# Kernel optimization log

Measured on AMD Instinct MI355X. Metric: run time of the kernel, lower is better.

Reference implementation:

```python
import jax, jax.numpy as jnp
import numpy as np

B, S, D, H, FF = 4, 2048, 512, 8, 2048
HD = D // H
SCALE = float(D) ** 0.5  # original scales by sqrt(embed_dim), not sqrt(head_dim)
EPS = 1e-5


def setup_inputs() -> dict:
    key = jax.random.key(0)
    ks = jax.random.split(key, 16)
    s_in = 1.0 / np.sqrt(D)
    s_ff = 1.0 / np.sqrt(FF)
    return {
        "embeddings": jax.random.normal(ks[0], (B, S, D), dtype=jnp.float32),
        "mask": jnp.ones((B, S), dtype=bool),
        # per-head Q/K/V projections stacked: [H, D, HD]
        "Wq": jax.random.uniform(ks[1], (H, D, HD), jnp.float32, -s_in, s_in),
        "bq": jax.random.uniform(ks[2], (H, HD), jnp.float32, -s_in, s_in),
        "Wk": jax.random.uniform(ks[3], (H, D, HD), jnp.float32, -s_in, s_in),
        "bk": jax.random.uniform(ks[4], (H, HD), jnp.float32, -s_in, s_in),
        "Wv": jax.random.uniform(ks[5], (H, D, HD), jnp.float32, -s_in, s_in),
        "bv": jax.random.uniform(ks[6], (H, HD), jnp.float32, -s_in, s_in),
        "Wc": jax.random.uniform(ks[7], (D, D), jnp.float32, -s_in, s_in),
        "bc": jax.random.uniform(ks[8], (D,), jnp.float32, -s_in, s_in),
        "W1": jax.random.uniform(ks[9], (D, FF), jnp.float32, -s_in, s_in),
        "b1": jax.random.uniform(ks[10], (FF,), jnp.float32, -s_in, s_in),
        "W2": jax.random.uniform(ks[11], (FF, D), jnp.float32, -s_ff, s_ff),
        "b2": jax.random.uniform(ks[12], (D,), jnp.float32, -s_ff, s_ff),
        "gamma": jnp.ones((D,), jnp.float32),
        "beta": jnp.zeros((D,), jnp.float32),
    }


def reference(embeddings, mask, Wq, bq, Wk, bk, Wv, bv, Wc, bc, W1, b1, W2, b2, gamma, beta):
    # Per-head projections batched into one einsum each: [B,H,S,HD]
    Q = jnp.einsum("bsd,hdf->bhsf", embeddings, Wq) + bq[:, None, :]
    K = jnp.einsum("bsd,hdf->bhsf", embeddings, Wk) + bk[:, None, :]
    V = jnp.einsum("bsd,hdf->bhsf", embeddings, Wv) + bv[:, None, :]
    # NOTE: the original computes a masked score tensor but then softmaxes the
    # UNMASKED scores (bug). We faithfully ignore the mask here.
    scores = jnp.einsum("bhsf,bhtf->bhst", Q, K) / SCALE  # [B,H,S,S]
    A = jax.nn.softmax(scores, axis=-1)
    Hh = jnp.einsum("bhst,bhtf->bhsf", A, V)  # [B,H,S,HD]
    # concat heads along feature dim (head h -> contiguous slice)
    Hcat = jnp.transpose(Hh, (0, 2, 1, 3)).reshape(B, S, D)
    Hp = Hcat @ Wc + bc
    # add & norm (dropout is identity at eval)
    res = Hp + embeddings
    mu = jnp.mean(res, axis=-1, keepdims=True)
    var = jnp.var(res, axis=-1, keepdims=True)
    Hn = (res - mu) / jnp.sqrt(var + EPS) * gamma + beta
    out = jax.nn.relu(Hn @ W1 + b1) @ W2 + b2  # no residual after FFN in original
    return out, mask
```

## Files before the change

### kernel.cpp

```cpp
#include <hip/hip_runtime.h>
#include <hip/hip_bf16.h>
#include <cstdint>
#include <cstddef>

typedef short  s16x8 __attribute__((ext_vector_type(8)));
typedef short  s16x4 __attribute__((ext_vector_type(4)));
typedef float  f32x4 __attribute__((ext_vector_type(4)));
typedef unsigned u32x2 __attribute__((ext_vector_type(2)));

static constexpr int Bb = 4, Ss = 2048, Dd = 512, Hh = 8, HDd = 64, FFf = 2048;
static constexpr int Mm = Bb * Ss;

__device__ __forceinline__ unsigned short f2bf(float f) {
  unsigned u = __float_as_uint(f);
  u += 0x7FFFu + ((u >> 16) & 1u);
  return (unsigned short)(u >> 16);
}

__device__ __forceinline__ unsigned cvt_pk_bf16(float lo, float hi) {
  unsigned r;
  asm("v_cvt_pk_bf16_f32 %0, %1, %2" : "=v"(r) : "v"(lo), "v"(hi));
  return r;
}

#define GLOAD_LDS16(gp, lp)                                                     \
  __builtin_amdgcn_global_load_lds((const __attribute__((address_space(1))) void*)(gp), \
                                   (__attribute__((address_space(3))) void*)(lp), 16, 0, 0)

__device__ __forceinline__ void xpose_tile(const float* __restrict__ in,
                                           unsigned short* __restrict__ out,
                                           int K, int N, int bx, int by, float (*t)[33]) {
  const int lx = threadIdx.x & 31, ly = threadIdx.x >> 5;
  const int n0 = bx * 32, k0 = by * 32;
#pragma unroll
  for (int r = 0; r < 4; ++r) t[ly + r * 8][lx] = in[(size_t)(k0 + ly + r * 8) * N + n0 + lx];
  __syncthreads();
#pragma unroll
  for (int r = 0; r < 4; ++r)
    out[(size_t)(n0 + ly + r * 8) * K + k0 + lx] = f2bf(t[lx][ly + r * 8]);
}

__global__ __launch_bounds__(256) void prep_all(
    const float* __restrict__ emb, const float* __restrict__ Wq, const float* __restrict__ Wk,
    const float* __restrict__ Wv, const float* __restrict__ Wc, const float* __restrict__ W1,
    const float* __restrict__ W2, unsigned short* __restrict__ embB,
    unsigned short* __restrict__ WtQKV, unsigned short* __restrict__ WtC,
    unsigned short* __restrict__ Wt1, unsigned short* __restrict__ Wt2,
    float* __restrict__ maskOut) {
  __shared__ float t[32][33];
  const int blk = blockIdx.x;
  if (blk < 4096) {
    const int i = blk * 256 + threadIdx.x;
    const float4 v = reinterpret_cast<const float4*>(emb)[i];
    s16x4 o; o[0] = f2bf(v.x); o[1] = f2bf(v.y); o[2] = f2bf(v.z); o[3] = f2bf(v.w);
    reinterpret_cast<s16x4*>(embB)[i] = o;
  } else if (blk < 4864) {
    const int b = blk - 4096;
    const int bx = b & 15, by = (b >> 4) & 1, z = b >> 5;
    const int sel = z >> 3, h = z & 7;
    const float* W = sel == 0 ? Wq : (sel == 1 ? Wk : Wv);
    const float* inb = W + (size_t)h * 512 * 64;
    unsigned short* outb = WtQKV + (size_t)sel * 512 * 512 + (size_t)h * 64 * 512;
    const int lx = threadIdx.x & 31, ly = threadIdx.x >> 5;
    const int d0 = bx * 32, f0 = by * 32;
#pragma unroll
    for (int r = 0; r < 4; ++r) t[ly + r * 8][lx] = inb[(size_t)(d0 + ly + r * 8) * 64 + f0 + lx];
    __syncthreads();
#pragma unroll
    for (int r = 0; r < 4; ++r)
      outb[(size_t)(f0 + ly + r * 8) * 512 + d0 + lx] = f2bf(t[lx][ly + r * 8]);
  } else if (blk < 5120) {
    const int b = blk - 4864;
    xpose_tile(Wc, WtC, 512, 512, b & 15, b >> 4, t);
  } else if (blk < 6144) {
    const int b = blk - 5120;
    xpose_tile(W1, Wt1, 512, 2048, b & 63, b >> 6, t);
  } else if (blk < 7168) {
    const int b = blk - 6144;
    xpose_tile(W2, Wt2, 2048, 512, b & 15, b >> 4, t);
  } else {
    const int i = (blk - 7168) * 256 + threadIdx.x;
    if (i < Bb * Ss) maskOut[i] = 1.0f;
  }
}

template<int EPI>
__global__ __launch_bounds__(256) void gemm_bt(
    const unsigned short* __restrict__ A, const unsigned short* __restrict__ Bt,
    const float* __restrict__ bias0, const float* __restrict__ bias1, const float* __restrict__ bias2,
    const float* __restrict__ addf, float* __restrict__ outF,
    unsigned short* __restrict__ outB0, unsigned short* __restrict__ outB1,
    unsigned short* __restrict__ outB2, int M, int N, int K) {
  __shared__ alignas(16) unsigned short As[2][128 * 32];
  __shared__ alignas(16) unsigned short Bs[2][128 * 32];
  const int tid = threadIdx.x;
  const int lane = tid & 63, wid = tid >> 6;
  const int wr = wid >> 1, wc = wid & 1;
  const int fr = lane & 15, kg = lane >> 4;
  const int m0 = blockIdx.y * 128, n0 = blockIdx.x * 128;

  const unsigned short* gA = A + (size_t)(m0 + (tid >> 2)) * K + ((tid & 3) << 3);
  const unsigned short* gB = Bt + (size_t)(n0 + (tid >> 2)) * K + ((tid & 3) << 3);

  auto STAGE = [&](int kt, int buf) {
    unsigned short* lA = &As[buf][wid * 512];
    unsigned short* lB = &Bs[buf][wid * 512];
    GLOAD_LDS16(gA + kt, lA);
    GLOAD_LDS16(gA + (size_t)64 * K + kt, lA + 2048);
    GLOAD_LDS16(gB + kt, lB);
    GLOAD_LDS16(gB + (size_t)64 * K + kt, lB + 2048);
  };

  f32x4 acc[4][4];
#pragma unroll
  for (int i = 0; i < 4; ++i)
#pragma unroll
    for (int j = 0; j < 4; ++j)
#pragma unroll
      for (int r = 0; r < 4; ++r) acc[i][j][r] = 0.f;

  STAGE(0, 0);
  const int nk = K >> 5;
  for (int ki = 0; ki < nk; ++ki) {
    const int cur = ki & 1;
    __builtin_amdgcn_s_barrier();
    if (ki + 1 < nk) {
      STAGE((ki + 1) << 5, cur ^ 1);
      asm volatile("s_waitcnt vmcnt(4)" ::: "memory");
    } else {
      asm volatile("s_waitcnt vmcnt(0)" ::: "memory");
    }
    __builtin_amdgcn_sched_barrier(0);
    __builtin_amdgcn_s_barrier();
    __builtin_amdgcn_sched_barrier(0);

    s16x8 af[4], bfv[4];
#pragma unroll
    for (int i = 0; i < 4; ++i)
      af[i] = *reinterpret_cast<const s16x8*>(&As[cur][(wr * 64 + i * 16 + fr) * 32 + kg * 8]);
#pragma unroll
    for (int i = 0; i < 4; ++i)
      bfv[i] = *reinterpret_cast<const s16x8*>(&Bs[cur][(wc * 64 + i * 16 + fr) * 32 + kg * 8]);
#pragma unroll
    for (int mi = 0; mi < 4; ++mi)
#pragma unroll
      for (int ni = 0; ni < 4; ++ni)
        acc[mi][ni] = __builtin_amdgcn_mfma_f32_16x16x32_bf16(af[mi], bfv[ni], acc[mi][ni], 0, 0, 0);
  }

#pragma unroll
  for (int mi = 0; mi < 4; ++mi)
#pragma unroll
    for (int ni = 0; ni < 4; ++ni)
#pragma unroll
      for (int r = 0; r < 4; ++r) {
        const int row = m0 + wr * 64 + mi * 16 + kg * 4 + r;
        const int col = n0 + wc * 64 + ni * 16 + fr;
        float v = acc[mi][ni][r];
        if constexpr (EPI == 0) {
          const int sel = col >> 9, c = col & 511;
          const float* bs = sel == 0 ? bias0 : (sel == 1 ? bias1 : bias2);
          v += bs[c];
          const int b = row >> 11, s = row & 2047;
          const int h = c >> 6, f = c & 63;
          if (sel == 0)
            outB0[((size_t)((b << 3) + h) * 2048 + s) * 64 + f] = f2bf(v);
          else if (sel == 1)
            outB1[((size_t)((b << 3) + h) * 2048 + s) * 64 + f] = f2bf(v);
          else
            outB2[((size_t)((b << 3) + h) * 64 + f) * 2048 + s] = f2bf(v);
        } else if constexpr (EPI == 1) {
          const size_t idx = (size_t)row * 512 + col;
          outF[idx] = v + bias0[col] + addf[idx];
        } else if constexpr (EPI == 2) {
          v += bias0[col];
          outB0[(size_t)row * 2048 + col] = f2bf(v > 0.f ? v : 0.f);
        } else {
          outF[(size_t)row * 512 + col] = v + bias0[col];
        }
      }
}

__global__ __launch_bounds__(256) void attn_kernel(const unsigned short* __restrict__ Q,
                                                   const unsigned short* __restrict__ Kx,
                                                   const unsigned short* __restrict__ V,
                                                   unsigned short* __restrict__ Hcat) {
  const int lane = threadIdx.x & 63, wid = threadIdx.x >> 6;
  const int fr = lane & 15, kg = lane >> 4;
  const int lin = blockIdx.x;
  const int xcd = lin & 7, idx = lin >> 3;
  const int bh = xcd * 4 + (idx & 3);
  const int qi = idx >> 2;
  const int b = bh >> 3, h = bh & 7;
  const int q0 = qi * 64 + wid * 16;
  const unsigned short* Qh = Q + (size_t)bh * Ss * HDd;
  const unsigned short* Kh = Kx + (size_t)bh * Ss * HDd;
  const unsigned short* Vh = V + (size_t)bh * HDd * Ss;

  __shared__ alignas(16) unsigned short Ks[2][64 * 64];
  __shared__ alignas(16) unsigned short Vs[64 * 64];
  __shared__ alignas(16) unsigned short P[4][16][72];

  const int srow = lane >> 3;
  const int scol = ((lane & 7) ^ srow) << 3;
  const unsigned short* gK0 = Kh + (size_t)(8 * (2 * wid + 0) + srow) * 64 + scol;
  const unsigned short* gK1 = Kh + (size_t)(8 * (2 * wid + 1) + srow) * 64 + scol;
  const unsigned short* gV0 = Vh + (size_t)(8 * (2 * wid + 0) + srow) * 2048 + scol;
  const unsigned short* gV1 = Vh + (size_t)(8 * (2 * wid + 1) + srow) * 2048 + scol;
  unsigned short* lK0a = &Ks[0][(2 * wid + 0) * 512];
  unsigned short* lK1a = &Ks[0][(2 * wid + 1) * 512];
  unsigned short* lK0b = &Ks[1][(2 * wid + 0) * 512];
  unsigned short* lK1b = &Ks[1][(2 * wid + 1) * 512];
  unsigned short* lV0 = &Vs[(2 * wid + 0) * 512];
  unsigned short* lV1 = &Vs[(2 * wid + 1) * 512];

  s16x8 bq[2];
#pragma unroll
  for (int kb = 0; kb < 2; ++kb)
    bq[kb] = *reinterpret_cast<const s16x8*>(&Qh[(size_t)(q0 + fr) * 64 + kb * 32 + kg * 8]);

  f32x4 o[4];
#pragma unroll
  for (int ct = 0; ct < 4; ++ct)
#pragma unroll
    for (int r = 0; r < 4; ++r) o[ct][r] = 0.f;
  float mr = -1e30f, lsum = 0.f;

  const float iscL = 1.4426950408889634f * 0.044194173824159216f;
  const int swz = (fr & 7) << 3;

  GLOAD_LDS16(gK0, lK0a);
  GLOAD_LDS16(gK1, lK1a);
  GLOAD_LDS16(gV0, lV0);
  GLOAD_LDS16(gV1, lV1);

#pragma unroll 1
  for (int t = 0; t < 32; ++t) {
    const int kt = t * 64;
    const int ktn = (kt + 64) & 2047;
    const unsigned short* KsC = Ks[t & 1];
    unsigned short* nK0 = (t & 1) ? lK0a : lK0b;
    unsigned short* nK1 = (t & 1) ? lK1a : lK1b;

    asm volatile("s_waitcnt vmcnt(2)" ::: "memory");
    __builtin_amdgcn_sched_barrier(0);
    __builtin_amdgcn_s_barrier();
    __builtin_amdgcn_sched_barrier(0);

    f32x4 sc[4];
#pragma unroll
    for (int ct = 0; ct < 4; ++ct)
#pragma unroll
      for (int r = 0; r < 4; ++r) sc[ct][r] = 0.f;
#pragma unroll
    for (int ct = 0; ct < 4; ++ct)
#pragma unroll
      for (int kb = 0; kb < 2; ++kb) {
        const s16x8 kf = *reinterpret_cast<const s16x8*>(
            &KsC[(ct * 16 + fr) * 64 + (((kg << 3) + (kb << 5)) ^ swz)]);
        sc[ct] = __builtin_amdgcn_mfma_f32_16x16x32_bf16(kf, bq[kb], sc[ct], 0, 0, 0);
      }

    GLOAD_LDS16(gK0 + (size_t)ktn * 64, nK0);
    GLOAD_LDS16(gK1 + (size_t)ktn * 64, nK1);

    float mxl;
    {
      const float a0 = fmaxf(fmaxf(sc[0][0], sc[0][1]), fmaxf(sc[0][2], sc[0][3]));
      const float a1 = fmaxf(fmaxf(sc[1][0], sc[1][1]), fmaxf(sc[1][2], sc[1][3]));
      const float a2 = fmaxf(fmaxf(sc[2][0], sc[2][1]), fmaxf(sc[2][2], sc[2][3]));
      const float a3 = fmaxf(fmaxf(sc[3][0], sc[3][1]), fmaxf(sc[3][2], sc[3][3]));
      mxl = fmaxf(fmaxf(a0, a1), fmaxf(a2, a3)) * iscL;
    }
    if (!__all(mxl <= mr + 8.0f)) {
      float mx = fmaxf(mxl, __shfl_xor(mxl, 16));
      mx = fmaxf(mx, __shfl_xor(mx, 32));
      const float mn = fmaxf(mr, mx);
      const float corr = exp2f(mr - mn);
      mr = mn;
      lsum *= corr;
      float corrq[4];
#pragma unroll
      for (int r = 0; r < 4; ++r) corrq[r] = __shfl(corr, kg * 4 + r);
#pragma unroll
      for (int ct = 0; ct < 4; ++ct)
#pragma unroll
        for (int r = 0; r < 4; ++r) o[ct][r] *= corrq[r];
    }

    float ps0 = 0.f, ps1 = 0.f;
#pragma unroll
    for (int ct = 0; ct < 4; ++ct) {
      float p0 = exp2f(__builtin_fmaf(sc[ct][0], iscL, -mr));
      float p1 = exp2f(__builtin_fmaf(sc[ct][1], iscL, -mr));
      float p2 = exp2f(__builtin_fmaf(sc[ct][2], iscL, -mr));
      float p3 = exp2f(__builtin_fmaf(sc[ct][3], iscL, -mr));
      ps0 += (p0 + p1);
      ps1 += (p2 + p3);
      u32x2 pk;
      pk[0] = cvt_pk_bf16(p0, p1);
      pk[1] = cvt_pk_bf16(p2, p3);
      *reinterpret_cast<u32x2*>(&P[wid][fr][ct * 16 + kg * 4]) = pk;
    }
    lsum += ps0 + ps1;

    asm volatile("s_waitcnt vmcnt(2)" ::: "memory");
    __builtin_amdgcn_sched_barrier(0);
    __builtin_amdgcn_s_barrier();
    __builtin_amdgcn_sched_barrier(0);

    const s16x8 pa0 = *reinterpret_cast<const s16x8*>(&P[wid][fr][kg * 8]);
    const s16x8 pa1 = *reinterpret_cast<const s16x8*>(&P[wid][fr][32 + kg * 8]);
#pragma unroll
    for (int ct = 0; ct < 4; ++ct) {
      const s16x8 bv0 = *reinterpret_cast<const s16x8*>(
          &Vs[(ct * 16 + fr) * 64 + (((kg << 3) + 0) ^ swz)]);
      o[ct] = __builtin_amdgcn_mfma_f32_16x16x32_bf16(pa0, bv0, o[ct], 0, 0, 0);
      const s16x8 bv1 = *reinterpret_cast<const s16x8*>(
          &Vs[(ct * 16 + fr) * 64 + (((kg << 3) + 32) ^ swz)]);
      o[ct] = __builtin_amdgcn_mfma_f32_16x16x32_bf16(pa1, bv1, o[ct], 0, 0, 0);
    }

    __builtin_amdgcn_s_barrier();
    __builtin_amdgcn_sched_barrier(0);
    GLOAD_LDS16(gV0 + ktn, lV0);
    GLOAD_LDS16(gV1 + ktn, lV1);
  }

  lsum += __shfl_xor(lsum, 16);
  lsum += __shfl_xor(lsum, 32);
  float invq[4];
#pragma unroll
  for (int r = 0; r < 4; ++r) invq[r] = 1.0f / __shfl(lsum, kg * 4 + r);
#pragma unroll
  for (int ct = 0; ct < 4; ++ct)
#pragma unroll
    for (int r = 0; r < 4; ++r) {
      const int qrow = q0 + kg * 4 + r;
      Hcat[(size_t)(b * Ss + qrow) * Dd + h * 64 + ct * 16 + fr] = f2bf(o[ct][r] * invq[r]);
    }
}

__global__ __launch_bounds__(256) void layernorm_k(const float* __restrict__ res,
                                                   const float* __restrict__ gamma,
                                                   const float* __restrict__ beta,
                                                   unsigned short* __restrict__ out) {
  const int lane = threadIdx.x & 63, wid = threadIdx.x >> 6;
  const int row = blockIdx.x * 4 + wid;
  const float* rp = res + (size_t)row * 512 + lane * 8;
  const float4 v0 = *reinterpret_cast<const float4*>(rp);
  const float4 v1 = *reinterpret_cast<const float4*>(rp + 4);
  float x[8] = {v0.x, v0.y, v0.z, v0.w, v1.x, v1.y, v1.z, v1.w};
  float s = 0.f, q = 0.f;
#pragma unroll
  for (int j = 0; j < 8; ++j) { s += x[j]; q += x[j] * x[j]; }
#pragma unroll
  for (int off = 32; off; off >>= 1) { s += __shfl_xor(s, off); q += __shfl_xor(q, off); }
  const float mean = s * (1.f / 512.f);
  const float var = q * (1.f / 512.f) - mean * mean;
  const float rstd = rsqrtf(var + 1e-5f);
  s16x8 o;
#pragma unroll
  for (int j = 0; j < 8; ++j) {
    const int c = lane * 8 + j;
    o[j] = f2bf((x[j] - mean) * rstd * gamma[c] + beta[c]);
  }
  *reinterpret_cast<s16x8*>(out + (size_t)row * 512 + lane * 8) = o;
}

extern "C" void kernel_launch(void* const* d_in, const int* in_sizes, int n_in,
                              void* d_out, int out_size, void* d_ws, size_t ws_size,
                              hipStream_t stream) {
  const float* emb = (const float*)d_in[0];
  const float* Wq = (const float*)d_in[2];
  const float* bq = (const float*)d_in[3];
  const float* Wk = (const float*)d_in[4];
  const float* bk = (const float*)d_in[5];
  const float* Wv = (const float*)d_in[6];
  const float* bv = (const float*)d_in[7];
  const float* Wc = (const float*)d_in[8];
  const float* bc = (const float*)d_in[9];
  const float* W1 = (const float*)d_in[10];
  const float* b1 = (const float*)d_in[11];
  const float* W2 = (const float*)d_in[12];
  const float* b2 = (const float*)d_in[13];
  const float* gamma = (const float*)d_in[14];
  const float* beta = (const float*)d_in[15];
  float* out = (float*)d_out;

  char* ws = (char*)d_ws;
  size_t off = 0;
  auto alloc = [&](size_t bytes) {
    char* p = ws + off;
    off = (off + bytes + 255) & ~(size_t)255;
    return p;
  };
  unsigned short* embB = (unsigned short*)alloc((size_t)Mm * Dd * 2);
  unsigned short* WtQKV = (unsigned short*)alloc((size_t)1536 * 512 * 2);
  unsigned short* WtC = (unsigned short*)alloc((size_t)512 * 512 * 2);
  unsigned short* Wt1 = (unsigned short*)alloc((size_t)2048 * 512 * 2);
  unsigned short* Wt2 = (unsigned short*)alloc((size_t)512 * 2048 * 2);
  unsigned short* Qb = (unsigned short*)alloc((size_t)Mm * Dd * 2);
  unsigned short* Kb = (unsigned short*)alloc((size_t)Mm * Dd * 2);
  unsigned short* Vt = (unsigned short*)alloc((size_t)Mm * Dd * 2);
  unsigned short* Hcat = (unsigned short*)alloc((size_t)Mm * Dd * 2);
  float* resF = (float*)alloc((size_t)Mm * Dd * 4);
  unsigned short* HnB = (unsigned short*)alloc((size_t)Mm * Dd * 2);
  unsigned short* G = Qb;

  prep_all<<<7200, 256, 0, stream>>>(emb, Wq, Wk, Wv, Wc, W1, W2,
                                     embB, WtQKV, WtC, Wt1, Wt2,
                                     out + (size_t)Mm * Dd);

  gemm_bt<0><<<dim3(12, 64), 256, 0, stream>>>(embB, WtQKV, bq, bk, bv, nullptr, nullptr,
                                               Qb, Kb, Vt, Mm, 1536, 512);
  attn_kernel<<<1024, 256, 0, stream>>>(Qb, Kb, Vt, Hcat);
  gemm_bt<1><<<dim3(4, 64), 256, 0, stream>>>(Hcat, WtC, bc, nullptr, nullptr, emb, resF,
                                              nullptr, nullptr, nullptr, Mm, 512, 512);
  layernorm_k<<<2048, 256, 0, stream>>>(resF, gamma, beta, HnB);
  gemm_bt<2><<<dim3(16, 64), 256, 0, stream>>>(HnB, Wt1, b1, nullptr, nullptr, nullptr, nullptr,
                                               G, nullptr, nullptr, Mm, 2048, 512);
  gemm_bt<3><<<dim3(4, 64), 256, 0, stream>>>(G, Wt2, b2, nullptr, nullptr, nullptr, out,
                                              nullptr, nullptr, nullptr, Mm, 512, 2048);
}
```

Before: 203.5 us.

## Process two query fragments per wave in attention to reuse K/V tiles

Each wave now handles 32 query rows (two 16-row fragments) instead of 16, so a block covers 128 queries and the grid is halved to 512 blocks. Each K and V fragment loaded from LDS is reused for two MFMAs, and the global-to-LDS traffic for K/V per query is halved. The cost is higher register pressure from doubled accumulators and score tiles, and fewer blocks (512 on a 256-CU device), which may reduce occupancy and latency hiding.

```diff
diff --git a/kernel.cpp b/kernel.cpp
--- a/kernel.cpp
+++ b/kernel.cpp
@@ -190,16 +190,16 @@
   const int lin = blockIdx.x;
   const int xcd = lin & 7, idx = lin >> 3;
   const int bh = xcd * 4 + (idx & 3);
-  const int qi = idx >> 2;
+  const int qi2 = idx >> 2;
   const int b = bh >> 3, h = bh & 7;
-  const int q0 = qi * 64 + wid * 16;
+  const int q0 = qi2 * 128 + wid * 32;
   const unsigned short* Qh = Q + (size_t)bh * Ss * HDd;
   const unsigned short* Kh = Kx + (size_t)bh * Ss * HDd;
   const unsigned short* Vh = V + (size_t)bh * HDd * Ss;
 
   __shared__ alignas(16) unsigned short Ks[2][64 * 64];
   __shared__ alignas(16) unsigned short Vs[64 * 64];
-  __shared__ alignas(16) unsigned short P[4][16][72];
+  __shared__ alignas(16) unsigned short P[4][2][16][72];
 
   const int srow = lane >> 3;
   const int scol = ((lane & 7) ^ srow) << 3;
@@ -214,17 +214,22 @@
   unsigned short* lV0 = &Vs[(2 * wid + 0) * 512];
   unsigned short* lV1 = &Vs[(2 * wid + 1) * 512];
 
-  s16x8 bq[2];
-#pragma unroll
-  for (int kb = 0; kb < 2; ++kb)
-    bq[kb] = *reinterpret_cast<const s16x8*>(&Qh[(size_t)(q0 + fr) * 64 + kb * 32 + kg * 8]);
-
-  f32x4 o[4];
-#pragma unroll
-  for (int ct = 0; ct < 4; ++ct)
-#pragma unroll
-    for (int r = 0; r < 4; ++r) o[ct][r] = 0.f;
-  float mr = -1e30f, lsum = 0.f;
+  s16x8 bq[2][2];
+#pragma unroll
+  for (int qf = 0; qf < 2; ++qf)
+#pragma unroll
+    for (int kb = 0; kb < 2; ++kb)
+      bq[qf][kb] = *reinterpret_cast<const s16x8*>(
+          &Qh[(size_t)(q0 + qf * 16 + fr) * 64 + kb * 32 + kg * 8]);
+
+  f32x4 o[2][4];
+#pragma unroll
+  for (int qf = 0; qf < 2; ++qf)
+#pragma unroll
+    for (int ct = 0; ct < 4; ++ct)
+#pragma unroll
+      for (int r = 0; r < 4; ++r) o[qf][ct][r] = 0.f;
+  float mr[2] = {-1e30f, -1e30f}, lsum[2] = {0.f, 0.f};
 
   const float iscL = 1.4426950408889634f * 0.044194173824159216f;
   const int swz = (fr & 7) << 3;
@@ -247,79 +252,89 @@
     __builtin_amdgcn_s_barrier();
     __builtin_amdgcn_sched_barrier(0);
 
-    f32x4 sc[4];
-#pragma unroll
-    for (int ct = 0; ct < 4; ++ct)
-#pragma unroll
-      for (int r = 0; r < 4; ++r) sc[ct][r] = 0.f;
+    f32x4 sc[2][4];
+#pragma unroll
+    for (int qf = 0; qf < 2; ++qf)
+#pragma unroll
+      for (int ct = 0; ct < 4; ++ct)
+#pragma unroll
+        for (int r = 0; r < 4; ++r) sc[qf][ct][r] = 0.f;
 #pragma unroll
     for (int ct = 0; ct < 4; ++ct)
 #pragma unroll
       for (int kb = 0; kb < 2; ++kb) {
         const s16x8 kf = *reinterpret_cast<const s16x8*>(
             &KsC[(ct * 16 + fr) * 64 + (((kg << 3) + (kb << 5)) ^ swz)]);
-        sc[ct] = __builtin_amdgcn_mfma_f32_16x16x32_bf16(kf, bq[kb], sc[ct], 0, 0, 0);
+        sc[0][ct] = __builtin_amdgcn_mfma_f32_16x16x32_bf16(kf, bq[0][kb], sc[0][ct], 0, 0, 0);
+        sc[1][ct] = __builtin_amdgcn_mfma_f32_16x16x32_bf16(kf, bq[1][kb], sc[1][ct], 0, 0, 0);
       }
 
     GLOAD_LDS16(gK0 + (size_t)ktn * 64, nK0);
     GLOAD_LDS16(gK1 + (size_t)ktn * 64, nK1);
 
-    float mxl;
-    {
-      const float a0 = fmaxf(fmaxf(sc[0][0], sc[0][1]), fmaxf(sc[0][2], sc[0][3]));
-      const float a1 = fmaxf(fmaxf(sc[1][0], sc[1][1]), fmaxf(sc[1][2], sc[1][3]));
-      const float a2 = fmaxf(fmaxf(sc[2][0], sc[2][1]), fmaxf(sc[2][2], sc[2][3]));
-      const float a3 = fmaxf(fmaxf(sc[3][0], sc[3][1]), fmaxf(sc[3][2], sc[3][3]));
-      mxl = fmaxf(fmaxf(a0, a1), fmaxf(a2, a3)) * iscL;
+#pragma unroll
+    for (int qf = 0; qf < 2; ++qf) {
+      float mxl;
+      {
+        const float a0 = fmaxf(fmaxf(sc[qf][0][0], sc[qf][0][1]), fmaxf(sc[qf][0][2], sc[qf][0][3]));
+        const float a1 = fmaxf(fmaxf(sc[qf][1][0], sc[qf][1][1]), fmaxf(sc[qf][1][2], sc[qf][1][3]));
+        const float a2 = fmaxf(fmaxf(sc[qf][2][0], sc[qf][2][1]), fmaxf(sc[qf][2][2], sc[qf][2][3]));
+        const float a3 = fmaxf(fmaxf(sc[qf][3][0], sc[qf][3][1]), fmaxf(sc[qf][3][2], sc[qf][3][3]));
+        mxl = fmaxf(fmaxf(a0, a1), fmaxf(a2, a3)) * iscL;
+      }
+      if (!__all(mxl <= mr[qf] + 8.0f)) {
+        float mx = fmaxf(mxl, __shfl_xor(mxl, 16));
+        mx = fmaxf(mx, __shfl_xor(mx, 32));
+        const float mn = fmaxf(mr[qf], mx);
+        const float corr = exp2f(mr[qf] - mn);
+        mr[qf] = mn;
+        lsum[qf] *= corr;
+        float corrq[4];
+#pragma unroll
+        for (int r = 0; r < 4; ++r) corrq[r] = __shfl(corr, kg * 4 + r);
+#pragma unroll
+        for (int ct = 0; ct < 4; ++ct)
+#pragma unroll
+          for (int r = 0; r < 4; ++r) o[qf][ct][r] *= corrq[r];
+      }
+
+      float ps0 = 0.f, ps1 = 0.f;
+#pragma unroll
+      for (int ct = 0; ct < 4; ++ct) {
+        float p0 = exp2f(__builtin_fmaf(sc[qf][ct][0], iscL, -mr[qf]));
+        float p1 = exp2f(__builtin_fmaf(sc[qf][ct][1], iscL, -mr[qf]));
+        float p2 = exp2f(__builtin_fmaf(sc[qf][ct][2], iscL, -mr[qf]));
+        float p3 = exp2f(__builtin_fmaf(sc[qf][ct][3], iscL, -mr[qf]));
+        ps0 += (p0 + p1);
+        ps1 += (p2 + p3);
+        u32x2 pk;
+        pk[0] = cvt_pk_bf16(p0, p1);
+        pk[1] = cvt_pk_bf16(p2, p3);
+        *reinterpret_cast<u32x2*>(&P[wid][qf][fr][ct * 16 + kg * 4]) = pk;
+      }
+      lsum[qf] += ps0 + ps1;
     }
-    if (!__all(mxl <= mr + 8.0f)) {
-      float mx = fmaxf(mxl, __shfl_xor(mxl, 16));
-      mx = fmaxf(mx, __shfl_xor(mx, 32));
-      const float mn = fmaxf(mr, mx);
-      const float corr = exp2f(mr - mn);
-      mr = mn;
-      lsum *= corr;
-      float corrq[4];
-#pragma unroll
-      for (int r = 0; r < 4; ++r) corrq[r] = __shfl(corr, kg * 4 + r);
-#pragma unroll
-      for (int ct = 0; ct < 4; ++ct)
-#pragma unroll
-        for (int r = 0; r < 4; ++r) o[ct][r] *= corrq[r];
+
+    asm volatile("s_waitcnt vmcnt(2)" ::: "memory");
+    __builtin_amdgcn_sched_barrier(0);
+    __builtin_amdgcn_s_barrier();
+    __builtin_amdgcn_sched_barrier(0);
+
+    s16x8 pa[2][2];
+#pragma unroll
+    for (int qf = 0; qf < 2; ++qf) {
+      pa[qf][0] = *reinterpret_cast<const s16x8*>(&P[wid][qf][fr][kg * 8]);
+      pa[qf][1] = *reinterpret_cast<const s16x8*>(&P[wid][qf][fr][32 + kg * 8]);
     }
-
-    float ps0 = 0.f, ps1 = 0.f;
-#pragma unroll
-    for (int ct = 0; ct < 4; ++ct) {
-      float p0 = exp2f(__builtin_fmaf(sc[ct][0], iscL, -mr));
-      float p1 = exp2f(__builtin_fmaf(sc[ct][1], iscL, -mr));
-      float p2 = exp2f(__builtin_fmaf(sc[ct][2], iscL, -mr));
-      float p3 = exp2f(__builtin_fmaf(sc[ct][3], iscL, -mr));
-      ps0 += (p0 + p1);
-      ps1 += (p2 + p3);
-      u32x2 pk;
-      pk[0] = cvt_pk_bf16(p0, p1);
-      pk[1] = cvt_pk_bf16(p2, p3);
-      *reinterpret_cast<u32x2*>(&P[wid][fr][ct * 16 + kg * 4]) = pk;
-    }
-    lsum += ps0 + ps1;
-
-    asm volatile("s_waitcnt vmcnt(2)" ::: "memory");
-    __builtin_amdgcn_sched_barrier(0);
-    __builtin_amdgcn_s_barrier();
-    __builtin_amdgcn_sched_barrier(0);
-
-    const s16x8 pa0 = *reinterpret_cast<const s16x8*>(&P[wid][fr][kg * 8]);
-    const s16x8 pa1 = *reinterpret_cast<const s16x8*>(&P[wid][fr][32 + kg * 8]);
-#pragma unroll
-    for (int ct = 0; ct < 4; ++ct) {
-      const s16x8 bv0 = *reinterpret_cast<const s16x8*>(
-          &Vs[(ct * 16 + fr) * 64 + (((kg << 3) + 0) ^ swz)]);
-      o[ct] = __builtin_amdgcn_mfma_f32_16x16x32_bf16(pa0, bv0, o[ct], 0, 0, 0);
-      const s16x8 bv1 = *reinterpret_cast<const s16x8*>(
-          &Vs[(ct * 16 + fr) * 64 + (((kg << 3) + 32) ^ swz)]);
-      o[ct] = __builtin_amdgcn_mfma_f32_16x16x32_bf16(pa1, bv1, o[ct], 0, 0, 0);
-    }
+#pragma unroll
+    for (int ct = 0; ct < 4; ++ct)
+#pragma unroll
+      for (int kb = 0; kb < 2; ++kb) {
+        const s16x8 bv = *reinterpret_cast<const s16x8*>(
+            &Vs[(ct * 16 + fr) * 64 + (((kg << 3) + (kb << 5)) ^ swz)]);
+        o[0][ct] = __builtin_amdgcn_mfma_f32_16x16x32_bf16(pa[0][kb], bv, o[0][ct], 0, 0, 0);
+        o[1][ct] = __builtin_amdgcn_mfma_f32_16x16x32_bf16(pa[1][kb], bv, o[1][ct], 0, 0, 0);
+      }
 
     __builtin_amdgcn_s_barrier();
     __builtin_amdgcn_sched_barrier(0);
@@ -327,18 +342,22 @@
     GLOAD_LDS16(gV1 + ktn, lV1);
   }
 
-  lsum += __shfl_xor(lsum, 16);
-  lsum += __shfl_xor(lsum, 32);
-  float invq[4];
-#pragma unroll
-  for (int r = 0; r < 4; ++r) invq[r] = 1.0f / __shfl(lsum, kg * 4 + r);
-#pragma unroll
-  for (int ct = 0; ct < 4; ++ct)
-#pragma unroll
-    for (int r = 0; r < 4; ++r) {
-      const int qrow = q0 + kg * 4 + r;
-      Hcat[(size_t)(b * Ss + qrow) * Dd + h * 64 + ct * 16 + fr] = f2bf(o[ct][r] * invq[r]);
-    }
+#pragma unroll
+  for (int qf = 0; qf < 2; ++qf) {
+    float ls = lsum[qf];
+    ls += __shfl_xor(ls, 16);
+    ls += __shfl_xor(ls, 32);
+    float invq[4];
+#pragma unroll
+    for (int r = 0; r < 4; ++r) invq[r] = 1.0f / __shfl(ls, kg * 4 + r);
+#pragma unroll
+    for (int ct = 0; ct < 4; ++ct)
+#pragma unroll
+      for (int r = 0; r < 4; ++r) {
+        const int qrow = q0 + qf * 16 + kg * 4 + r;
+        Hcat[(size_t)(b * Ss + qrow) * Dd + h * 64 + ct * 16 + fr] = f2bf(o[qf][ct][r] * invq[r]);
+      }
+  }
 }
 
 __global__ __launch_bounds__(256) void layernorm_k(const float* __restrict__ res,
@@ -414,7 +433,7 @@
 
   gemm_bt<0><<<dim3(12, 64), 256, 0, stream>>>(embB, WtQKV, bq, bk, bv, nullptr, nullptr,
                                                Qb, Kb, Vt, Mm, 1536, 512);
-  attn_kernel<<<1024, 256, 0, stream>>>(Qb, Kb, Vt, Hcat);
+  attn_kernel<<<512, 256, 0, stream>>>(Qb, Kb, Vt, Hcat);
   gemm_bt<1><<<dim3(4, 64), 256, 0, stream>>>(Hcat, WtC, bc, nullptr, nullptr, emb, resF,
                                               nullptr, nullptr, nullptr, Mm, 512, 512);
   layernorm_k<<<2048, 256, 0, stream>>>(resF, gamma, beta, HnB);
```

Result: slower. 208.3 us (+2.4%).
